# Optimization experiments

Measured on AMD Instinct MI355X. Metric: run time of the kernel, lower is better.

## Reference

```python
import jax, jax.numpy as jnp
import numpy as np

# Model config (matches init_kwargs)
L_F, DELTA_F, L_S, DELTA_S = 1, 1, 32, 16
HIDDEN = 32       # SSM state dim H
GRU_H = 64        # slow-branch GRU hidden
N_GRU = 4
B, T = 4, 32768


def setup_inputs() -> dict:
    key = jax.random.key(0)
    ks = jax.random.split(key, 13)
    def nrm(k, shape, s=0.05):
        return jax.random.normal(k, shape, dtype=jnp.float32) * s
    return {
        "x": jax.random.normal(ks[0], (B, T), dtype=jnp.float32),
        # SlowBranch params
        "fc_in_w": nrm(ks[1], (GRU_H, 1), 0.3),
        "fc_in_b": nrm(ks[2], (GRU_H,)),
        "gru_wih": nrm(ks[3], (N_GRU, 3 * GRU_H, GRU_H), 0.1),
        "gru_whh": nrm(ks[4], (N_GRU, 3 * GRU_H, GRU_H), 0.1),
        "gru_bih": nrm(ks[5], (N_GRU, 3 * GRU_H)),
        "gru_bhh": nrm(ks[6], (N_GRU, 3 * GRU_H)),
        "out_fc_w": nrm(ks[7], (2 * HIDDEN, GRU_H), 0.1),
        "out_fc_b": nrm(ks[8], (2 * HIDDEN,)),
        # Fast branch params (F_IN: 1->H, F_OUT: H->1)
        "fin_w": nrm(ks[9], (HIDDEN, 1), 0.3),
        "fin_b": nrm(ks[10], (HIDDEN,)),
        "fout_w": nrm(ks[11], (1, HIDDEN), 0.1),
        "fout_b": nrm(ks[12], (1,)),
    }


def _gru_layer(xs, Wih, Whh, bih, bhh):
    """Torch-convention GRU layer. xs: (N, L, H_in) -> (N, L, H)."""
    H = Whh.shape[1]
    # Precompute input-side gate pre-activations: (N, L, 3H)
    xp = jnp.einsum('nlh,gh->nlg', xs, Wih) + bih
    def step(h, xt):
        gh = h @ Whh.T + bhh                       # (N, 3H)
        ir, iz, inew = jnp.split(xt, 3, axis=-1)
        hr, hz, hnew = jnp.split(gh, 3, axis=-1)
        r = jax.nn.sigmoid(ir + hr)
        z = jax.nn.sigmoid(iz + hz)
        n = jnp.tanh(inew + r * hnew)
        h = (1.0 - z) * n + z * h
        return h, h
    h0 = jnp.zeros((xs.shape[0], H), xs.dtype)
    _, ys = jax.lax.scan(step, h0, jnp.swapaxes(xp, 0, 1))  # (L, N, H)
    return jnp.swapaxes(ys, 0, 1)


def reference(x, fc_in_w, fc_in_b, gru_wih, gru_whh, gru_bih, gru_bhh,
              out_fc_w, out_fc_b, fin_w, fin_b, fout_w, fout_b):
    Bsz, Tlen = x.shape
    num_slow = (Tlen - L_S) // DELTA_S + 1

    frame_idx = jnp.arange(num_slow)[:, None] * DELTA_S + jnp.arange(L_S)[None, :]
    x_s = x[:, frame_idx].reshape(Bsz * num_slow, L_S, 1)      # (N, L_s, 1)
    h = jax.nn.relu(x_s * fc_in_w[:, 0] + fc_in_b)             # (N, L_s, GRU_H)
    for l in range(gru_wih.shape[0]):
        h = _gru_layer(h, gru_wih[l], gru_whh[l], gru_bih[l], gru_bhh[l])
    eps = h[:, -1, :] @ out_fc_w.T + out_fc_b                  # (N, 2H)
    eps = eps.reshape(Bsz, num_slow, 2 * HIDDEN)
    A_slow = jax.nn.sigmoid(eps[..., :HIDDEN])                 # (B, S, H)
    g_slow = eps[..., HIDDEN:]                                 # (B, S, H)

    # ---- Fast branch: per-sample diagonal linear SSM scan ----
    delta = DELTA_S // DELTA_F
    idx = jnp.clip(jnp.arange(Tlen) // delta - 1, 0, num_slow - 1)  # (T,)
    A_t = A_slow[:, idx, :]                                    # (B, T, H)
    u_t = (x[..., None] * fin_w[:, 0] + fin_b) * g_slow[:, idx, :]  # (B, T, H)

    def step(hc, inp):
        A, u = inp
        hn = A * hc + u
        return hn, hn
    h0 = jnp.zeros((Bsz, HIDDEN), x.dtype)
    _, h_all = jax.lax.scan(step, h0,
                            (jnp.swapaxes(A_t, 0, 1), jnp.swapaxes(u_t, 0, 1)))
    # h_all: (T, B, H); F_OUT applied to every state
    return jnp.einsum('tbh,h->bt', h_all, fout_w[0]) + fout_b[0]   # (B, T)
```

## Files before the change

kernel.cpp:

```cpp
#include <hip/hip_runtime.h>
#include <hip/hip_bf16.h>

typedef __bf16 bf16x8 __attribute__((ext_vector_type(8)));
typedef short short8 __attribute__((ext_vector_type(8)));
typedef float f32x4 __attribute__((ext_vector_type(4)));
typedef unsigned short ushort_t;

#define T_LEN 32768
#define B_SZ 4
#define NSLOW 2047
#define NSEQ (B_SZ * NSLOW)
#define GH 64
#define G3 192
#define NL 4
#define HID 32
#define NCH 256
#define L2E 1.44269504088896341f

#define OFF_X    0
#define OFF_FCW  131072
#define OFF_FCB  131136
#define OFF_WIH  131200
#define OFF_WHH  180352
#define OFF_BIH  229504
#define OFF_BHH  230272
#define OFF_OFW  231040
#define OFF_OFB  235136
#define OFF_FINW 235200
#define OFF_FINB 235232
#define OFF_FOW  235264
#define OFF_FOB  235296
#define CONV_TOTAL 235297
#define CONV_PAD_BYTES 470656

static __device__ __forceinline__ float bf2f(ushort_t u) {
    union { unsigned u; float f; } c; c.u = ((unsigned)u) << 16; return c.f;
}
static __device__ __forceinline__ ushort_t f2bf(float f) {
    union { float f; unsigned u; } c; c.f = f;
    unsigned r = (c.u + 0x7FFFu + ((c.u >> 16) & 1u)) >> 16;
    return (ushort_t)r;
}
static __device__ __forceinline__ unsigned pk2bf(float a, float b) {
    float2 f; f.x = a; f.y = b;
    __hip_bfloat162 h = __float22bfloat162_rn(f);
    unsigned u;
    __builtin_memcpy(&u, &h, 4);
    return u;
}
static __device__ __forceinline__ f32x4 mfma16(short8 a, short8 b, f32x4 c) {
    return __builtin_amdgcn_mfma_f32_16x16x32_bf16(
        __builtin_bit_cast(bf16x8, a), __builtin_bit_cast(bf16x8, b), c, 0, 0, 0);
}
static __device__ __forceinline__ int xoff(int t, int kb, int seq) {
    return ((((t << 3) + kb) << 4) + (seq ^ (kb & 7))) << 3;
}
static __device__ __forceinline__ short8 load_frag_scaled(const ushort_t* p, float s) {
    uint4 r = *(const uint4*)p;
    unsigned aa[4] = {r.x, r.y, r.z, r.w};
    short8 o;
#pragma unroll
    for (int i = 0; i < 4; ++i) {
        o[2 * i]     = (short)f2bf(bf2f((ushort_t)(aa[i] & 0xffffu)) * s);
        o[2 * i + 1] = (short)f2bf(bf2f((ushort_t)(aa[i] >> 16)) * s);
    }
    return o;
}

__global__ __launch_bounds__(64) void detect_kernel(const ushort_t* __restrict__ x,
                                                    int* __restrict__ flag)
{
    int lane = threadIdx.x;
    int cnt = 0;
#pragma unroll
    for (int i = 0; i < 4; ++i) {
        ushort_t u = x[lane * 4 + i];
        int e = (u >> 7) & 0xFF;
        if (e >= 80 && e <= 141) cnt++;
    }
#pragma unroll
    for (int d = 1; d < 64; d <<= 1) cnt += __shfl_xor(cnt, d, 64);
    if (lane == 0) *flag = (cnt >= 224) ? 1 : 0;
}

struct Ptrs13 { const void* p[13]; };

__global__ __launch_bounds__(256) void convert_kernel(Ptrs13 ptrs,
                                                      const int* __restrict__ flag,
                                                      ushort_t* __restrict__ dst)
{
    const int offs[14] = {OFF_X, OFF_FCW, OFF_FCB, OFF_WIH, OFF_WHH, OFF_BIH,
                          OFF_BHH, OFF_OFW, OFF_OFB, OFF_FINW, OFF_FINB,
                          OFF_FOW, OFF_FOB, CONV_TOTAL};
    const bool isbf = (*flag != 0);
    for (int idx = blockIdx.x * 256 + threadIdx.x; idx < CONV_TOTAL;
         idx += gridDim.x * 256) {
        int s = 0;
#pragma unroll
        for (int j = 1; j < 13; ++j) if (idx >= offs[j]) s = j;
        int k = idx - offs[s];
        ushort_t v = isbf ? ((const ushort_t*)ptrs.p[s])[k]
                          : f2bf(((const float*)ptrs.p[s])[k]);
        dst[idx] = v;
    }
}

__global__ __launch_bounds__(256) void gru_kernel(
    const ushort_t* __restrict__ x, const ushort_t* __restrict__ fcw,
    const ushort_t* __restrict__ fcb, const ushort_t* __restrict__ wih,
    const ushort_t* __restrict__ whh, const ushort_t* __restrict__ bih,
    const ushort_t* __restrict__ bhh, const ushort_t* __restrict__ ofw,
    const ushort_t* __restrict__ ofb, float* __restrict__ Aslow,
    float* __restrict__ gslow)
{
    __shared__ short8 Xs8[4096];
    short* Xs = (short*)Xs8;
    const int tid = threadIdx.x;
    const int w = tid >> 6, lane = tid & 63;
    const int q = lane >> 4, m = lane & 15;
    const int jb = w * 16;
    const int n0 = blockIdx.x * 16;

#pragma unroll 1
    for (int ii = 0; ii < 16; ++ii) {
        int cid = ii * 256 + tid;
        int seq = cid & 15, kb = (cid >> 4) & 7, t = cid >> 7;
        int n = n0 + seq; if (n > NSEQ - 1) n = NSEQ - 1;
        int b = n / NSLOW, s = n - b * NSLOW;
        float xv = bf2f(x[b * T_LEN + s * 16 + t]);
        short8 v;
#pragma unroll
        for (int i = 0; i < 8; ++i) {
            int g = kb * 8 + i;
            float h = fmaf(xv, bf2f(fcw[g]), bf2f(fcb[g]));
            h = h > 0.f ? h : 0.f;
            v[i] = (short)f2bf(h);
        }
        Xs8[xoff(t, kb, seq) >> 3] = v;
    }

    const int col0 = jb + 4 * q;
    const int kbw = (col0 >> 3);
    const int wsub = (col0 & 7);
    const int kofs = q * 8;
    const int wbase0 = ((kbw << 4) + (m ^ (kbw & 7))) * 8 + wsub;

    float hc[4];
#pragma unroll 1
    for (int l = 0; l < NL; ++l) {
        const ushort_t* wl = wih + l * G3 * GH;
        const ushort_t* ul = whh + l * G3 * GH;
        short8 wR0 = load_frag_scaled(wl + (0 * 64 + jb + m) * 64 + kofs, -L2E);
        short8 wR1 = load_frag_scaled(wl + (0 * 64 + jb + m) * 64 + 32 + kofs, -L2E);
        short8 wZ0 = load_frag_scaled(wl + (1 * 64 + jb + m) * 64 + kofs, -L2E);
        short8 wZ1 = load_frag_scaled(wl + (1 * 64 + jb + m) * 64 + 32 + kofs, -L2E);
        short8 wN0 = load_frag_scaled(wl + (2 * 64 + jb + m) * 64 + kofs, 2.f * L2E);
        short8 wN1 = load_frag_scaled(wl + (2 * 64 + jb + m) * 64 + 32 + kofs, 2.f * L2E);
        short8 uR0 = load_frag_scaled(ul + (0 * 64 + jb + m) * 64 + kofs, -L2E);
        short8 uR1 = load_frag_scaled(ul + (0 * 64 + jb + m) * 64 + 32 + kofs, -L2E);
        short8 uZ0 = load_frag_scaled(ul + (1 * 64 + jb + m) * 64 + kofs, -L2E);
        short8 uZ1 = load_frag_scaled(ul + (1 * 64 + jb + m) * 64 + 32 + kofs, -L2E);
        short8 uN0 = load_frag_scaled(ul + (2 * 64 + jb + m) * 64 + kofs, 2.f * L2E);
        short8 uN1 = load_frag_scaled(ul + (2 * 64 + jb + m) * 64 + 32 + kofs, 2.f * L2E);

        float bR[4], bZ[4], bNX[4], bNH[4];
#pragma unroll
        for (int i = 0; i < 4; ++i) {
            int c = col0 + i;
            bR[i]  = -L2E * (bf2f(bih[l * G3 + c]) + bf2f(bhh[l * G3 + c]));
            bZ[i]  = -L2E * (bf2f(bih[l * G3 + 64 + c]) + bf2f(bhh[l * G3 + 64 + c]));
            bNX[i] = 2.f * L2E * bf2f(bih[l * G3 + 128 + c]);
            bNH[i] = 2.f * L2E * bf2f(bhh[l * G3 + 128 + c]);
        }

        hc[0] = hc[1] = hc[2] = hc[3] = 0.f;

        __syncthreads();
        int iA = xoff(0, q, m) >> 3;
        int iB = xoff(0, 4 + q, m) >> 3;
        short8 bx0 = Xs8[iA];
        short8 bx1 = Xs8[iB];
        int wb = wbase0;

#pragma unroll 1
        for (int t = 0; t < 32; ++t) {
            __syncthreads();
            short8 bh0 = bx0, bh1 = bx1;
            if (t > 0) {
                bh0 = Xs8[iA - 128];
                bh1 = Xs8[iB - 128];
            }
            short8 nx0 = bx0, nx1 = bx1;
            if (t < 31) {
                nx0 = Xs8[iA + 128];
                nx1 = Xs8[iB + 128];
            }
            f32x4 aR  = {bR[0], bR[1], bR[2], bR[3]};
            f32x4 aZ  = {bZ[0], bZ[1], bZ[2], bZ[3]};
            f32x4 aNX = {bNX[0], bNX[1], bNX[2], bNX[3]};
            f32x4 aNH = {bNH[0], bNH[1], bNH[2], bNH[3]};
            aR  = mfma16(wR0, bx0, aR);  aR  = mfma16(wR1, bx1, aR);
            aZ  = mfma16(wZ0, bx0, aZ);  aZ  = mfma16(wZ1, bx1, aZ);
            aNX = mfma16(wN0, bx0, aNX); aNX = mfma16(wN1, bx1, aNX);
            if (t > 0) {
                aR  = mfma16(uR0, bh0, aR);  aR  = mfma16(uR1, bh1, aR);
                aZ  = mfma16(uZ0, bh0, aZ);  aZ  = mfma16(uZ1, bh1, aZ);
                aNH = mfma16(uN0, bh0, aNH); aNH = mfma16(uN1, bh1, aNH);
            }
#pragma unroll
            for (int i = 0; i < 4; ++i) {
                float r = __builtin_amdgcn_rcpf(1.f + __builtin_amdgcn_exp2f(aR[i]));
                float z = __builtin_amdgcn_rcpf(1.f + __builtin_amdgcn_exp2f(aZ[i]));
                float yp = fmaf(r, aNH[i], aNX[i]);
                float nn = fmaf(-2.f,
                    __builtin_amdgcn_rcpf(1.f + __builtin_amdgcn_exp2f(yp)), 1.f);
                hc[i] = fmaf(z, hc[i] - nn, nn);
            }
            unsigned lo = pk2bf(hc[0], hc[1]);
            unsigned hi = pk2bf(hc[2], hc[3]);
            *(uint2*)(Xs + wb) = make_uint2(lo, hi);
            bx0 = nx0; bx1 = nx1;
            iA += 128; iB += 128; wb += 1024;
        }
    }

    __syncthreads();
    short8 aL0 = Xs8[xoff(31, q, m) >> 3];
    short8 aL1 = Xs8[xoff(31, 4 + q, m) >> 3];
    float sc = (w < 2) ? -L2E : 1.f;
    short8 o0 = load_frag_scaled(ofw + (jb + m) * 64 + kofs, sc);
    short8 o1 = load_frag_scaled(ofw + (jb + m) * 64 + 32 + kofs, sc);
    f32x4 aE = {bf2f(ofb[col0]) * sc, bf2f(ofb[col0 + 1]) * sc,
                bf2f(ofb[col0 + 2]) * sc, bf2f(ofb[col0 + 3]) * sc};
    aE = mfma16(o0, aL0, aE);
    aE = mfma16(o1, aL1, aE);
    int n = n0 + m;
    if (w < 2) {
        f32x4 v;
#pragma unroll
        for (int i = 0; i < 4; ++i)
            v[i] = __builtin_amdgcn_rcpf(1.f + __builtin_amdgcn_exp2f(aE[i]));
        *(f32x4*)(Aslow + n * HID + col0) = v;
    } else {
        *(f32x4*)(gslow + n * HID + (col0 - 32)) = aE;
    }
}

__global__ __launch_bounds__(256) void pass1_kernel(
    const ushort_t* __restrict__ x, const float* __restrict__ Aslow,
    const float* __restrict__ gslow, const ushort_t* __restrict__ finw,
    const ushort_t* __restrict__ finb, float* __restrict__ P,
    float* __restrict__ S)
{
    int gt = blockIdx.x * 256 + threadIdx.x;
    int h = gt & 31, c = (gt >> 5) & 255, b = gt >> 13;
    float fw = bf2f(finw[h]), fb = bf2f(finb[h]);
    float Pv = 1.f, Sv = 0.f;
    int t0 = c * 128;
#pragma unroll 1
    for (int seg = 0; seg < 8; ++seg) {
        int sidx = (t0 >> 4) + seg - 1;
        if (sidx < 0) sidx = 0;
        if (sidx > NSLOW - 1) sidx = NSLOW - 1;
        float A = Aslow[(b * NSLOW + sidx) * HID + h];
        float g = gslow[(b * NSLOW + sidx) * HID + h];
        float fwg = fw * g, fbg = fb * g;
        const uint4* px = (const uint4*)(x + b * T_LEN + t0 + seg * 16);
        uint4 ra = px[0], rb = px[1];
        unsigned xa[8] = {ra.x, ra.y, ra.z, ra.w, rb.x, rb.y, rb.z, rb.w};
#pragma unroll
        for (int j = 0; j < 8; ++j) {
            float x0 = bf2f((ushort_t)(xa[j] & 0xffffu));
            float x1 = bf2f((ushort_t)(xa[j] >> 16));
            Sv = fmaf(A, Sv, fmaf(x0, fwg, fbg));
            Sv = fmaf(A, Sv, fmaf(x1, fwg, fbg));
        }
        float A2 = A * A, A4 = A2 * A2, A8 = A4 * A4;
        Pv *= A8 * A8;
    }
    P[(b * HID + h) * NCH + c] = Pv;
    S[(b * HID + h) * NCH + c] = Sv;
}

__global__ __launch_bounds__(128) void scan_kernel(
    const float* __restrict__ P, const float* __restrict__ S,
    float* __restrict__ Hpre)
{
    int tid = threadIdx.x;
    const float4* p4 = (const float4*)(P + tid * NCH);
    const float4* s4 = (const float4*)(S + tid * NCH);
    float* hp = Hpre + tid * NCH;
    float hr = 0.f;
#pragma unroll 1
    for (int c = 0; c < NCH / 4; ++c) {
        float4 pv = p4[c], sv = s4[c];
        hp[4 * c + 0] = hr; hr = fmaf(pv.x, hr, sv.x);
        hp[4 * c + 1] = hr; hr = fmaf(pv.y, hr, sv.y);
        hp[4 * c + 2] = hr; hr = fmaf(pv.z, hr, sv.z);
        hp[4 * c + 3] = hr; hr = fmaf(pv.w, hr, sv.w);
    }
}

__global__ __launch_bounds__(256) void pass2_kernel(
    const ushort_t* __restrict__ x, const float* __restrict__ Aslow,
    const float* __restrict__ gslow, const float* __restrict__ Hpre,
    const ushort_t* __restrict__ finw, const ushort_t* __restrict__ finb,
    const ushort_t* __restrict__ fow, const ushort_t* __restrict__ fob,
    const int* __restrict__ flag, void* __restrict__ outv)
{
    int wv = blockIdx.x * 4 + (threadIdx.x >> 6);
    int lane = threadIdx.x & 63;
    int half = lane >> 5, h = lane & 31;
    int pair = wv * 2 + half;
    int b = pair >> 8, c = pair & 255;
    const bool isbf = (*flag != 0);
    ushort_t* outb = (ushort_t*)outv;
    float* outf = (float*)outv;
    float hv = Hpre[(b * HID + h) * NCH + c];
    float fw = bf2f(finw[h]), fb = bf2f(finb[h]);
    float wo = bf2f(fow[h]), ob = bf2f(fob[0]);
    int t0 = c * 128;
#pragma unroll 1
    for (int blk = 0; blk < 4; ++blk) {
        float ykeep = 0.f;
        float A = 0.f, fwg = 0.f, fbg = 0.f;
#pragma unroll
        for (int tt = 0; tt < 32; ++tt) {
            int t = t0 + blk * 32 + tt;
            if ((tt & 15) == 0) {
                int sidx = (t >> 4) - 1;
                if (sidx < 0) sidx = 0;
                A = Aslow[(b * NSLOW + sidx) * HID + h];
                float g = gslow[(b * NSLOW + sidx) * HID + h];
                fwg = fw * g; fbg = fb * g;
            }
            float xv = bf2f(x[b * T_LEN + t]);
            hv = fmaf(A, hv, fmaf(xv, fwg, fbg));
            float y = hv * wo;
            y += __shfl_xor(y, 1, 64);
            y += __shfl_xor(y, 2, 64);
            y += __shfl_xor(y, 4, 64);
            y += __shfl_xor(y, 8, 64);
            y += __shfl_xor(y, 16, 64);
            if (tt == h) ykeep = y + ob;
        }
        int oidx = b * T_LEN + t0 + blk * 32 + h;
        if (isbf) outb[oidx] = f2bf(ykeep);
        else      outf[oidx] = ykeep;
    }
}

extern "C" void kernel_launch(void* const* d_in, const int* in_sizes, int n_in,
                              void* d_out, int out_size, void* d_ws, size_t ws_size,
                              hipStream_t stream)
{
    ushort_t* cv = (ushort_t*)d_ws;
    const ushort_t* x    = cv + OFF_X;
    const ushort_t* fcw  = cv + OFF_FCW;
    const ushort_t* fcb  = cv + OFF_FCB;
    const ushort_t* wih  = cv + OFF_WIH;
    const ushort_t* whh  = cv + OFF_WHH;
    const ushort_t* bih  = cv + OFF_BIH;
    const ushort_t* bhh  = cv + OFF_BHH;
    const ushort_t* ofw  = cv + OFF_OFW;
    const ushort_t* ofb  = cv + OFF_OFB;
    const ushort_t* finw = cv + OFF_FINW;
    const ushort_t* finb = cv + OFF_FINB;
    const ushort_t* fow  = cv + OFF_FOW;
    const ushort_t* fob  = cv + OFF_FOB;

    float* Aslow = (float*)((char*)d_ws + CONV_PAD_BYTES);
    float* gslow = Aslow + 8192 * 32;
    float* P     = gslow + 8192 * 32;
    float* S     = P + 4 * 32 * NCH;
    float* Hpre  = S + 4 * 32 * NCH;
    int*   flag  = (int*)(Hpre + 4 * 32 * NCH);

    Ptrs13 ptrs;
    for (int i = 0; i < 13; ++i) ptrs.p[i] = d_in[i];

    detect_kernel<<<dim3(1), dim3(64), 0, stream>>>((const ushort_t*)d_in[0], flag);
    convert_kernel<<<dim3(920), dim3(256), 0, stream>>>(ptrs, flag, cv);
    gru_kernel<<<dim3(512), dim3(256), 0, stream>>>(
        x, fcw, fcb, wih, whh, bih, bhh, ofw, ofb, Aslow, gslow);
    pass1_kernel<<<dim3(128), dim3(256), 0, stream>>>(
        x, Aslow, gslow, finw, finb, P, S);
    scan_kernel<<<dim3(1), dim3(128), 0, stream>>>(P, S, Hpre);
    pass2_kernel<<<dim3(128), dim3(256), 0, stream>>>(
        x, Aslow, gslow, Hpre, finw, finb, fow, fob, flag, d_out);
}
```

Measured before the change: 211.8 us.

## Fold dtype detection into convert, software-pipeline GRU input projection, tune bounds

Removes the separate detect kernel: each convert block now computes the bf16/fp32 detection flag itself from the first 256 input elements, which saves one launch. The GRU time loop now computes the input-side projection for step t+1 after the hidden state for step t has been written. Only the recurrent MFMAs remain on the serial dependency chain between barriers, and the t==0 special case is peeled out. It also adds a launch_bounds occupancy hint of 2 to the GRU kernel and unrolls the tiny scan loop by 8, at the cost of higher register pressure.

Measured after the change: 191.4 us. 9.6% less time.

```diff
diff --git a/kernel.cpp b/kernel.cpp
--- a/kernel.cpp
+++ b/kernel.cpp
@@ -67,32 +67,30 @@
     return o;
 }
 
-__global__ __launch_bounds__(64) void detect_kernel(const ushort_t* __restrict__ x,
-                                                    int* __restrict__ flag)
-{
-    int lane = threadIdx.x;
-    int cnt = 0;
-#pragma unroll
-    for (int i = 0; i < 4; ++i) {
-        ushort_t u = x[lane * 4 + i];
+struct Ptrs13 { const void* p[13]; };
+
+__global__ __launch_bounds__(256) void convert_kernel(Ptrs13 ptrs,
+                                                      int* __restrict__ flag,
+                                                      ushort_t* __restrict__ dst)
+{
+    __shared__ int scnt;
+    if (threadIdx.x == 0) scnt = 0;
+    __syncthreads();
+    {
+        ushort_t u = ((const ushort_t*)ptrs.p[0])[threadIdx.x];
         int e = (u >> 7) & 0xFF;
-        if (e >= 80 && e <= 141) cnt++;
-    }
-#pragma unroll
-    for (int d = 1; d < 64; d <<= 1) cnt += __shfl_xor(cnt, d, 64);
-    if (lane == 0) *flag = (cnt >= 224) ? 1 : 0;
-}
-
-struct Ptrs13 { const void* p[13]; };
-
-__global__ __launch_bounds__(256) void convert_kernel(Ptrs13 ptrs,
-                                                      const int* __restrict__ flag,
-                                                      ushort_t* __restrict__ dst)
-{
+        int ok = (e >= 80 && e <= 141) ? 1 : 0;
+#pragma unroll
+        for (int d = 1; d < 64; d <<= 1) ok += __shfl_xor(ok, d, 64);
+        if ((threadIdx.x & 63) == 0) atomicAdd(&scnt, ok);
+    }
+    __syncthreads();
+    const bool isbf = (scnt >= 224);
+    if (blockIdx.x == 0 && threadIdx.x == 0) *flag = isbf ? 1 : 0;
+
     const int offs[14] = {OFF_X, OFF_FCW, OFF_FCB, OFF_WIH, OFF_WHH, OFF_BIH,
                           OFF_BHH, OFF_OFW, OFF_OFB, OFF_FINW, OFF_FINB,
                           OFF_FOW, OFF_FOB, CONV_TOTAL};
-    const bool isbf = (*flag != 0);
     for (int idx = blockIdx.x * 256 + threadIdx.x; idx < CONV_TOTAL;
          idx += gridDim.x * 256) {
         int s = 0;
@@ -105,7 +103,7 @@
     }
 }
 
-__global__ __launch_bounds__(256) void gru_kernel(
+__global__ __launch_bounds__(256, 2) void gru_kernel(
     const ushort_t* __restrict__ x, const ushort_t* __restrict__ fcw,
     const ushort_t* __restrict__ fcb, const ushort_t* __restrict__ wih,
     const ushort_t* __restrict__ whh, const ushort_t* __restrict__ bih,
@@ -163,14 +161,14 @@
         short8 uN0 = load_frag_scaled(ul + (2 * 64 + jb + m) * 64 + kofs, 2.f * L2E);
         short8 uN1 = load_frag_scaled(ul + (2 * 64 + jb + m) * 64 + 32 + kofs, 2.f * L2E);
 
-        float bR[4], bZ[4], bNX[4], bNH[4];
+        f32x4 bRv, bZv, bNXv, bNHv;
 #pragma unroll
         for (int i = 0; i < 4; ++i) {
             int c = col0 + i;
-            bR[i]  = -L2E * (bf2f(bih[l * G3 + c]) + bf2f(bhh[l * G3 + c]));
-            bZ[i]  = -L2E * (bf2f(bih[l * G3 + 64 + c]) + bf2f(bhh[l * G3 + 64 + c]));
-            bNX[i] = 2.f * L2E * bf2f(bih[l * G3 + 128 + c]);
-            bNH[i] = 2.f * L2E * bf2f(bhh[l * G3 + 128 + c]);
+            bRv[i]  = -L2E * (bf2f(bih[l * G3 + c]) + bf2f(bhh[l * G3 + c]));
+            bZv[i]  = -L2E * (bf2f(bih[l * G3 + 64 + c]) + bf2f(bhh[l * G3 + 64 + c]));
+            bNXv[i] = 2.f * L2E * bf2f(bih[l * G3 + 128 + c]);
+            bNHv[i] = 2.f * L2E * bf2f(bhh[l * G3 + 128 + c]);
         }
 
         hc[0] = hc[1] = hc[2] = hc[3] = 0.f;
@@ -178,48 +176,61 @@
         __syncthreads();
         int iA = xoff(0, q, m) >> 3;
         int iB = xoff(0, 4 + q, m) >> 3;
-        short8 bx0 = Xs8[iA];
-        short8 bx1 = Xs8[iB];
         int wb = wbase0;
 
+        short8 cx0 = Xs8[iA], cx1 = Xs8[iB];
+        short8 nx0 = Xs8[iA + 128], nx1 = Xs8[iB + 128];
+        f32x4 xR = bRv, xZ = bZv, xN = bNXv;
+        xR = mfma16(wR0, cx0, xR); xR = mfma16(wR1, cx1, xR);
+        xZ = mfma16(wZ0, cx0, xZ); xZ = mfma16(wZ1, cx1, xZ);
+        xN = mfma16(wN0, cx0, xN); xN = mfma16(wN1, cx1, xN);
+#pragma unroll
+        for (int i = 0; i < 4; ++i) {
+            float r = __builtin_amdgcn_rcpf(1.f + __builtin_amdgcn_exp2f(xR[i]));
+            float z = __builtin_amdgcn_rcpf(1.f + __builtin_amdgcn_exp2f(xZ[i]));
+            float yp = fmaf(r, bNHv[i], xN[i]);
+            float nn = fmaf(-2.f,
+                __builtin_amdgcn_rcpf(1.f + __builtin_amdgcn_exp2f(yp)), 1.f);
+            hc[i] = fmaf(z, hc[i] - nn, nn);
+        }
+        *(uint2*)(Xs + wb) = make_uint2(pk2bf(hc[0], hc[1]), pk2bf(hc[2], hc[3]));
+        xR = bRv; xZ = bZv; xN = bNXv;
+        xR = mfma16(wR0, nx0, xR); xR = mfma16(wR1, nx1, xR);
+        xZ = mfma16(wZ0, nx0, xZ); xZ = mfma16(wZ1, nx1, xZ);
+        xN = mfma16(wN0, nx0, xN); xN = mfma16(wN1, nx1, xN);
+        iA += 128; iB += 128; wb += 1024;
+
 #pragma unroll 1
-        for (int t = 0; t < 32; ++t) {
+        for (int t = 1; t < 32; ++t) {
             __syncthreads();
-            short8 bh0 = bx0, bh1 = bx1;
-            if (t > 0) {
-                bh0 = Xs8[iA - 128];
-                bh1 = Xs8[iB - 128];
+            short8 bh0 = Xs8[iA - 128];
+            short8 bh1 = Xs8[iB - 128];
+            short8 px0, px1;
+            if (t < 31) {
+                px0 = Xs8[iA + 128];
+                px1 = Xs8[iB + 128];
             }
-            short8 nx0 = bx0, nx1 = bx1;
-            if (t < 31) {
-                nx0 = Xs8[iA + 128];
-                nx1 = Xs8[iB + 128];
-            }
-            f32x4 aR  = {bR[0], bR[1], bR[2], bR[3]};
-            f32x4 aZ  = {bZ[0], bZ[1], bZ[2], bZ[3]};
-            f32x4 aNX = {bNX[0], bNX[1], bNX[2], bNX[3]};
-            f32x4 aNH = {bNH[0], bNH[1], bNH[2], bNH[3]};
-            aR  = mfma16(wR0, bx0, aR);  aR  = mfma16(wR1, bx1, aR);
-            aZ  = mfma16(wZ0, bx0, aZ);  aZ  = mfma16(wZ1, bx1, aZ);
-            aNX = mfma16(wN0, bx0, aNX); aNX = mfma16(wN1, bx1, aNX);
-            if (t > 0) {
-                aR  = mfma16(uR0, bh0, aR);  aR  = mfma16(uR1, bh1, aR);
-                aZ  = mfma16(uZ0, bh0, aZ);  aZ  = mfma16(uZ1, bh1, aZ);
-                aNH = mfma16(uN0, bh0, aNH); aNH = mfma16(uN1, bh1, aNH);
-            }
+            f32x4 aR = xR, aZ = xZ, aNH = bNHv;
+            aR  = mfma16(uR0, bh0, aR);  aR  = mfma16(uR1, bh1, aR);
+            aZ  = mfma16(uZ0, bh0, aZ);  aZ  = mfma16(uZ1, bh1, aZ);
+            aNH = mfma16(uN0, bh0, aNH); aNH = mfma16(uN1, bh1, aNH);
 #pragma unroll
             for (int i = 0; i < 4; ++i) {
                 float r = __builtin_amdgcn_rcpf(1.f + __builtin_amdgcn_exp2f(aR[i]));
                 float z = __builtin_amdgcn_rcpf(1.f + __builtin_amdgcn_exp2f(aZ[i]));
-                float yp = fmaf(r, aNH[i], aNX[i]);
+                float yp = fmaf(r, aNH[i], xN[i]);
                 float nn = fmaf(-2.f,
                     __builtin_amdgcn_rcpf(1.f + __builtin_amdgcn_exp2f(yp)), 1.f);
                 hc[i] = fmaf(z, hc[i] - nn, nn);
             }
-            unsigned lo = pk2bf(hc[0], hc[1]);
-            unsigned hi = pk2bf(hc[2], hc[3]);
-            *(uint2*)(Xs + wb) = make_uint2(lo, hi);
-            bx0 = nx0; bx1 = nx1;
+            *(uint2*)(Xs + wb) =
+                make_uint2(pk2bf(hc[0], hc[1]), pk2bf(hc[2], hc[3]));
+            if (t < 31) {
+                xR = bRv; xZ = bZv; xN = bNXv;
+                xR = mfma16(wR0, px0, xR); xR = mfma16(wR1, px1, xR);
+                xZ = mfma16(wZ0, px0, xZ); xZ = mfma16(wZ1, px1, xZ);
+                xN = mfma16(wN0, px0, xN); xN = mfma16(wN1, px1, xN);
+            }
             iA += 128; iB += 128; wb += 1024;
         }
     }
@@ -291,7 +302,7 @@
     const float4* s4 = (const float4*)(S + tid * NCH);
     float* hp = Hpre + tid * NCH;
     float hr = 0.f;
-#pragma unroll 1
+#pragma unroll 8
     for (int c = 0; c < NCH / 4; ++c) {
         float4 pv = p4[c], sv = s4[c];
         hp[4 * c + 0] = hr; hr = fmaf(pv.x, hr, sv.x);
@@ -379,7 +390,6 @@
     Ptrs13 ptrs;
     for (int i = 0; i < 13; ++i) ptrs.p[i] = d_in[i];
 
-    detect_kernel<<<dim3(1), dim3(64), 0, stream>>>((const ushort_t*)d_in[0], flag);
     convert_kernel<<<dim3(920), dim3(256), 0, stream>>>(ptrs, flag, cv);
     gru_kernel<<<dim3(512), dim3(256), 0, stream>>>(
         x, fcw, fcb, wih, whh, bih, bhh, ofw, ofb, Aslow, gslow);
```
